# Kernel tuning notes

Measured on AMD Instinct MI355X. Metric: run time of the kernel, lower is better.

## Reference

```python
import jax, jax.numpy as jnp
import numpy as np

N_NODES = 100000
N_EDGES = 1200000
IN_FEATS = 64
OUT_FEATS = 64


def setup_inputs() -> dict:
    key = jax.random.key(0)
    k1, k2, k3, k4 = jax.random.split(key, 4)
    feature = jax.random.normal(k1, (N_NODES, IN_FEATS), dtype=jnp.float32)
    edge_src = jax.random.randint(k2, (N_EDGES,), 0, N_NODES, dtype=jnp.int32)
    edge_dst = jax.random.randint(k3, (N_EDGES,), 0, N_NODES, dtype=jnp.int32)
    # xavier_normal_ init for linear weight (fan_in=fan_out=64)
    std = float(np.sqrt(2.0 / (IN_FEATS + OUT_FEATS)))
    W = jax.random.normal(k4, (OUT_FEATS, IN_FEATS), dtype=jnp.float32) * std
    b = jnp.zeros((OUT_FEATS,), dtype=jnp.float32)
    return {"feature": feature, "edge_src": edge_src, "edge_dst": edge_dst, "W": W, "b": b}


def reference(feature, edge_src, edge_dst, W, b):
    # copy_src: gather source-node features per edge, then mean-reduce by dst.
    msgs = feature[edge_src]                                   # [E, d_in]
    summed = jax.ops.segment_sum(msgs, edge_dst, num_segments=N_NODES)  # [N, d_in]
    deg = jax.ops.segment_sum(jnp.ones((edge_src.shape[0],), feature.dtype),
                              edge_dst, num_segments=N_NODES)  # [N]
    h = summed / jnp.maximum(deg, 1.0)[:, None]                # mean; 0 for isolated nodes
    # apply_nodes: linear + activation
    h = jnp.einsum("nd,od->no", h, W) + b
    return jax.nn.relu(h)
```

## Files before the change

### kernel.cpp

```cpp
#include <hip/hip_runtime.h>


typedef __attribute__((ext_vector_type(8))) short short8;
typedef __attribute__((ext_vector_type(4))) float floatx4;

constexpr int kNodes = 100000;
constexpr int kEdges = 1200000;

constexpr int kBuckets = 1024;
constexpr int kBucketNodes = 98;

constexpr int kBinBlocks = 256;
constexpr int kEdgesPerBlock = 4688;
constexpr int kEPT = (kEdgesPerBlock + 1023) / 1024;

constexpr int kCap = 2048;
constexpr int kAccStride = 68;

constexpr int kWsFeat   = 0;
constexpr int kWsOff    = 3200000;
constexpr int kWsBinned = kWsOff + kBinBlocks * (kBuckets + 1);

__device__ __forceinline__ unsigned bf16rne(float f) {
  unsigned u = __float_as_uint(f);
  return (u + 0x7fffu + ((u >> 16) & 1u)) >> 16;
}

__global__ __launch_bounds__(1024) void gcn_build(
    const float* __restrict__ feat,
    const int* __restrict__ src, const int* __restrict__ dst,
    int* __restrict__ ws) {
  uint2* fb16 = (uint2*)(ws + kWsFeat);
  int* offT   = ws + kWsOff;
  int* binned = ws + kWsBinned;

  __shared__ int lhist[kBuckets];
  __shared__ int lcur[kBuckets];
  __shared__ int wsum[16];

  const int tid = threadIdx.x;
  lhist[tid] = 0;
  __syncthreads();

  const int e0 = blockIdx.x * kEdgesPerBlock;
  const int cnt = min(kEdgesPerBlock, kEdges - e0);
  int es[kEPT], ebk[kEPT], edl[kEPT];
  #pragma unroll
  for (int k = 0; k < kEPT; ++k) {
    const int j = tid + k * 1024;
    if (j < cnt) {
      es[k] = src[e0 + j];
      const int d = dst[e0 + j];
      const int bk = d / kBucketNodes;
      ebk[k] = bk;
      edl[k] = d - bk * kBucketNodes;
      atomicAdd(&lhist[bk], 1);
    }
  }

  const int t = blockIdx.x * 1024 + tid;
  for (int i = t; i < kNodes * 16; i += kBinBlocks * 1024) {
    const float* fr = feat + (size_t)(i >> 4) * 64 + (i & 15);
    uint2 p;
    p.x = bf16rne(fr[0])  | (bf16rne(fr[16]) << 16);
    p.y = bf16rne(fr[32]) | (bf16rne(fr[48]) << 16);
    fb16[i] = p;
  }
  __syncthreads();

  const int own = lhist[tid];
  const int wv = tid >> 6, ln = tid & 63;
  int sc = own;
  #pragma unroll
  for (int off = 1; off < 64; off <<= 1) {
    const int v = __shfl_up(sc, off, 64);
    if (ln >= off) sc += v;
  }
  if (ln == 63) wsum[wv] = sc;
  __syncthreads();
  if (tid < 64) {
    int tw = (tid < 16) ? wsum[tid] : 0;
    #pragma unroll
    for (int off = 1; off < 16; off <<= 1) {
      const int v = __shfl_up(tw, off, 64);
      if (tid >= off) tw += v;
    }
    if (tid < 16) wsum[tid] = tw;
  }
  __syncthreads();
  const int excl = sc - own + (wv ? wsum[wv - 1] : 0);
  lcur[tid] = excl;
  offT[blockIdx.x * (kBuckets + 1) + tid] = excl;
  if (tid == 0) offT[blockIdx.x * (kBuckets + 1) + kBuckets] = cnt;
  __syncthreads();

  int* myBin = binned + blockIdx.x * kEdgesPerBlock;
  #pragma unroll
  for (int k = 0; k < kEPT; ++k) {
    const int j = tid + k * 1024;
    if (j < cnt) {
      const int pos = atomicAdd(&lcur[ebk[k]], 1);
      myBin[pos] = es[k] | (edl[k] << 17);
    }
  }
}

__global__ __launch_bounds__(1024, 8) void gcn_aggregate(
    const int*   __restrict__ ws_in,
    const float* __restrict__ W,
    const float* __restrict__ b,
    float*       __restrict__ out) {
  const uint2* fb16 = (const uint2*)(ws_in + kWsFeat);
  const int* offT   = ws_in + kWsOff;
  const int* binned = ws_in + kWsBinned;

  __shared__ __align__(16) char uShared[112 * 72 * 2];
  __shared__ __align__(16) int accum[kBucketNodes * kAccStride];
  __shared__ int    lofs[129];
  __shared__ int    lcur[128];
  __shared__ int    slotR[65];
  __shared__ int    runL[kBinBlocks + 1];
  __shared__ int    runG[kBinBlocks];
  __shared__ int    ssm[kBinBlocks];
  __shared__ ushort Wb16[64 * 64];
  __shared__ float  bsh[64];
  int*    lsrc  = (int*)uShared;
  ushort* hsAll = (ushort*)uShared;

  const int tid = threadIdx.x;
  const int bkt = blockIdx.x;

  if (tid < 128) lcur[tid] = 0;
  for (int i = tid; i < 4096; i += 1024) Wb16[i] = (ushort)bf16rne(W[i]);
  if (tid < 64) bsh[tid] = b[tid];

  if (tid < kBinBlocks) {
    const int o0 = offT[tid * (kBuckets + 1) + bkt];
    const int o1 = offT[tid * (kBuckets + 1) + bkt + 1];
    ssm[tid] = o1 - o0;
    runG[tid] = tid * kEdgesPerBlock + o0;
  }
  __syncthreads();
  if (tid < 64) {
    const int base = tid * 4;
    const int v0 = ssm[base], v1 = ssm[base + 1];
    const int v2 = ssm[base + 2], v3 = ssm[base + 3];
    const int p1 = v0 + v1, p2 = p1 + v2, tot = p2 + v3;
    int sc = tot;
    #pragma unroll
    for (int off = 1; off < 64; off <<= 1) {
      const int v = __shfl_up(sc, off, 64);
      if (tid >= off) sc += v;
    }
    const int ex = sc - tot;
    runL[base]     = ex;
    runL[base + 1] = ex + v0;
    runL[base + 2] = ex + p1;
    runL[base + 3] = ex + p2;
    if (tid == 63) runL[kBinBlocks] = sc;
  }
  __syncthreads();

  int sz = runL[kBinBlocks];
  if (sz > kCap) sz = kCap;

  auto mapRead = [&](int j) -> unsigned {
    int lo = 0, hi = kBinBlocks;
    #pragma unroll
    for (int it = 0; it < 8; ++it) {
      const int mid = (lo + hi) >> 1;
      if (runL[mid] <= j) lo = mid; else hi = mid;
    }
    return (unsigned)binned[runG[lo] + (j - runL[lo])];
  };

  const int j0 = tid, j1 = tid + 1024;
  const bool va = j0 < sz, vb = j1 < sz;
  unsigned ea = 0, eb = 0;
  if (va) { ea = mapRead(j0); atomicAdd(&lcur[ea >> 17], 1); }
  if (vb) { eb = mapRead(j1); atomicAdd(&lcur[eb >> 17], 1); }
  __syncthreads();

  if (tid < 64) {
    const int a  = lcur[tid * 2];
    const int b2 = lcur[tid * 2 + 1];
    int s = a + b2;
    #pragma unroll
    for (int off = 1; off < 64; off <<= 1) {
      const int v = __shfl_up(s, off, 64);
      if (tid >= off) s += v;
    }
    const int ex1 = s - b2;
    const int ex0 = ex1 - a;
    lofs[tid * 2]     = ex0;
    lofs[tid * 2 + 1] = ex1;
    lcur[tid * 2]     = ex0;
    lcur[tid * 2 + 1] = ex1;
    if (tid == 63) lofs[128] = s;
  }
  __syncthreads();

  if (va) { const int p = atomicAdd(&lcur[ea >> 17], 1); lsrc[p] = (int)ea; }
  if (vb) { const int p = atomicAdd(&lcur[eb >> 17], 1); lsrc[p] = (int)eb; }
  if (tid < 64) {
    const int tgt = (sz * tid) >> 6;
    int lo = 0, hi = kBucketNodes;
    #pragma unroll
    for (int it = 0; it < 7; ++it) {
      const int mid = (lo + hi) >> 1;
      if (lofs[mid] < tgt) lo = mid + 1; else hi = mid;
    }
    slotR[tid] = lo;
  }
  if (tid == 64) slotR[64] = kBucketNodes;
  __syncthreads();

  const int wave = tid >> 6;
  const int lane = tid & 63;
  const int g = lane >> 4;
  const int c = lane & 15;
  {
    const int slot = wave * 4 + g;
    int r = slotR[slot];
    const int rEnd = slotR[slot + 1];
    if (r < rEnd) {
      int j = lofs[r];
      const int jE = lofs[rEnd];
      int jN = lofs[r + 1];
      float a0 = 0.f, a1 = 0.f, a2 = 0.f, a3 = 0.f;
      unsigned e = (j < jE) ? (unsigned)lsrc[j] : 0u;
      uint2 v = fb16[(size_t)(e & 0x1FFFF) * 16 + c];
      while (j < jE) {
        while (j >= jN) {
          int* rp = accum + r * kAccStride + c;
          rp[0]  = __float_as_int(a0);
          rp[16] = __float_as_int(a1);
          rp[32] = __float_as_int(a2);
          rp[48] = __float_as_int(a3);
          a0 = a1 = a2 = a3 = 0.f;
          ++r; jN = lofs[r + 1];
        }
        const int jn = j + 1;
        const unsigned e2 = (jn < jE) ? (unsigned)lsrc[jn] : 0u;
        const uint2 v2 = fb16[(size_t)(e2 & 0x1FFFF) * 16 + c];
        a0 += __uint_as_float(v.x << 16);
        a1 += __uint_as_float(v.x & 0xffff0000u);
        a2 += __uint_as_float(v.y << 16);
        a3 += __uint_as_float(v.y & 0xffff0000u);
        v = v2; e = e2; j = jn;
      }
      while (r < rEnd) {
        int* rp = accum + r * kAccStride + c;
        rp[0]  = __float_as_int(a0);
        rp[16] = __float_as_int(a1);
        rp[32] = __float_as_int(a2);
        rp[48] = __float_as_int(a3);
        a0 = a1 = a2 = a3 = 0.f;
        ++r;
      }
    }
  }
  __syncthreads();

  {
    const int nd = tid >> 3;
    const int ch = tid & 7;
    if (nd < kBucketNodes) {
      const int dg = lofs[nd + 1] - lofs[nd];
      const float inv = 1.0f / (float)(dg > 1 ? dg : 1);
      const int* arow = accum + nd * kAccStride + ch * 8;
      const int4 pa = *(const int4*)(arow);
      const int4 pb = *(const int4*)(arow + 4);
      unsigned h0 = bf16rne(__int_as_float(pa.x) * inv);
      unsigned h1 = bf16rne(__int_as_float(pa.y) * inv);
      unsigned h2 = bf16rne(__int_as_float(pa.z) * inv);
      unsigned h3 = bf16rne(__int_as_float(pa.w) * inv);
      unsigned h4 = bf16rne(__int_as_float(pb.x) * inv);
      unsigned h5 = bf16rne(__int_as_float(pb.y) * inv);
      unsigned h6 = bf16rne(__int_as_float(pb.z) * inv);
      unsigned h7 = bf16rne(__int_as_float(pb.w) * inv);
      uint4 pk;
      pk.x = h0 | (h1 << 16);
      pk.y = h2 | (h3 << 16);
      pk.z = h4 | (h5 << 16);
      pk.w = h6 | (h7 << 16);
      *(uint4*)(hsAll + nd * 72 + ch * 8) = pk;
    } else {
      if (nd < 112) *(uint4*)(hsAll + nd * 72 + ch * 8) =
          make_uint4(0u, 0u, 0u, 0u);
    }
  }
  __syncthreads();

  if (tid < 448) {
    const int w8   = tid >> 6;
    const int ln   = tid & 63;
    const int quad = ln >> 4;
    const int col  = ln & 15;
    const int n0 = bkt * kBucketNodes;

    const short8 af0 = *reinterpret_cast<const short8*>(
        hsAll + (w8 * 16 + col) * 72 + 0 * 32 + quad * 8);
    const short8 af1 = *reinterpret_cast<const short8*>(
        hsAll + (w8 * 16 + col) * 72 + 1 * 32 + quad * 8);

    #pragma unroll
    for (int ob = 0; ob < 4; ++ob) {
      const short8 bf0 = *reinterpret_cast<const short8*>(
          Wb16 + (ob * 16 + col) * 64 + 0 * 32 + quad * 8);
      const short8 bf1 = *reinterpret_cast<const short8*>(
          Wb16 + (ob * 16 + col) * 64 + 1 * 32 + quad * 8);
      floatx4 acc = {0.f, 0.f, 0.f, 0.f};
      acc = __builtin_amdgcn_mfma_f32_16x16x32_bf16(af0, bf0, acc, 0, 0, 0);
      acc = __builtin_amdgcn_mfma_f32_16x16x32_bf16(af1, bf1, acc, 0, 0, 0);

      const int o = ob * 16 + col;
      const float bo = bsh[o];
      #pragma unroll
      for (int r = 0; r < 4; ++r) {
        const int local = w8 * 16 + quad * 4 + r;
        const int node = n0 + local;
        if (local < kBucketNodes && node < kNodes) {
          const float v = acc[r] + bo;
          out[(size_t)node * 64 + o] = v > 0.0f ? v : 0.0f;
        }
      }
    }
  }
}

extern "C" void kernel_launch(void* const* d_in, const int* in_sizes, int n_in,
                              void* d_out, int out_size, void* d_ws, size_t ws_size,
                              hipStream_t stream) {
  const float* feature  = (const float*)d_in[0];
  const int*   edge_src = (const int*)  d_in[1];
  const int*   edge_dst = (const int*)  d_in[2];
  const float* W        = (const float*)d_in[3];
  const float* b        = (const float*)d_in[4];

  float* out = (float*)d_out;
  int*   ws  = (int*)d_ws;

  gcn_build<<<kBinBlocks, 1024, 0, stream>>>(feature, edge_src, edge_dst, ws);
  gcn_aggregate<<<kBuckets, 1024, 0, stream>>>(ws, W, b, out);
}
```

Before: 132.9 us.

## Transpose bucket offset table and unroll per-node gather by four edges

The per-block bucket offset table is stored bucket-major instead of block-major, so the aggregate kernel's 256 threads read contiguous offsets for their bucket instead of striding by 1025 ints. The aggregation loop becomes a per-node loop that issues four independent feature gathers at a time into separate accumulators, replacing the single-edge software-pipelined loop. This aims for more memory-level parallelism on the gathers and coalesced offset reads, at the cost of more registers and a scalar remainder loop for low-degree nodes.

```diff
diff --git a/kernel.cpp b/kernel.cpp
--- a/kernel.cpp
+++ b/kernel.cpp
@@ -19,7 +19,7 @@
 
 constexpr int kWsFeat   = 0;
 constexpr int kWsOff    = 3200000;
-constexpr int kWsBinned = kWsOff + kBinBlocks * (kBuckets + 1);
+constexpr int kWsBinned = kWsOff + (kBuckets + 1) * kBinBlocks;
 
 __device__ __forceinline__ unsigned bf16rne(float f) {
   unsigned u = __float_as_uint(f);
@@ -31,7 +31,7 @@
     const int* __restrict__ src, const int* __restrict__ dst,
     int* __restrict__ ws) {
   uint2* fb16 = (uint2*)(ws + kWsFeat);
-  int* offT   = ws + kWsOff;
+  int* offTT  = ws + kWsOff;
   int* binned = ws + kWsBinned;
 
   __shared__ int lhist[kBuckets];
@@ -90,8 +90,8 @@
   __syncthreads();
   const int excl = sc - own + (wv ? wsum[wv - 1] : 0);
   lcur[tid] = excl;
-  offT[blockIdx.x * (kBuckets + 1) + tid] = excl;
-  if (tid == 0) offT[blockIdx.x * (kBuckets + 1) + kBuckets] = cnt;
+  offTT[tid * kBinBlocks + blockIdx.x] = excl;
+  if (tid == 0) offTT[kBuckets * kBinBlocks + blockIdx.x] = cnt;
   __syncthreads();
 
   int* myBin = binned + blockIdx.x * kEdgesPerBlock;
@@ -111,7 +111,7 @@
     const float* __restrict__ b,
     float*       __restrict__ out) {
   const uint2* fb16 = (const uint2*)(ws_in + kWsFeat);
-  const int* offT   = ws_in + kWsOff;
+  const int* offTT  = ws_in + kWsOff;
   const int* binned = ws_in + kWsBinned;
 
   __shared__ __align__(16) char uShared[112 * 72 * 2];
@@ -135,8 +135,8 @@
   if (tid < 64) bsh[tid] = b[tid];
 
   if (tid < kBinBlocks) {
-    const int o0 = offT[tid * (kBuckets + 1) + bkt];
-    const int o1 = offT[tid * (kBuckets + 1) + bkt + 1];
+    const int o0 = offTT[bkt * kBinBlocks + tid];
+    const int o1 = offTT[(bkt + 1) * kBinBlocks + tid];
     ssm[tid] = o1 - o0;
     runG[tid] = tid * kEdgesPerBlock + o0;
   }
@@ -221,43 +221,56 @@
   const int c = lane & 15;
   {
     const int slot = wave * 4 + g;
-    int r = slotR[slot];
     const int rEnd = slotR[slot + 1];
-    if (r < rEnd) {
-      int j = lofs[r];
-      const int jE = lofs[rEnd];
-      int jN = lofs[r + 1];
-      float a0 = 0.f, a1 = 0.f, a2 = 0.f, a3 = 0.f;
-      unsigned e = (j < jE) ? (unsigned)lsrc[j] : 0u;
-      uint2 v = fb16[(size_t)(e & 0x1FFFF) * 16 + c];
-      while (j < jE) {
-        while (j >= jN) {
-          int* rp = accum + r * kAccStride + c;
-          rp[0]  = __float_as_int(a0);
-          rp[16] = __float_as_int(a1);
-          rp[32] = __float_as_int(a2);
-          rp[48] = __float_as_int(a3);
-          a0 = a1 = a2 = a3 = 0.f;
-          ++r; jN = lofs[r + 1];
-        }
-        const int jn = j + 1;
-        const unsigned e2 = (jn < jE) ? (unsigned)lsrc[jn] : 0u;
-        const uint2 v2 = fb16[(size_t)(e2 & 0x1FFFF) * 16 + c];
-        a0 += __uint_as_float(v.x << 16);
-        a1 += __uint_as_float(v.x & 0xffff0000u);
-        a2 += __uint_as_float(v.y << 16);
-        a3 += __uint_as_float(v.y & 0xffff0000u);
-        v = v2; e = e2; j = jn;
+    for (int r = slotR[slot]; r < rEnd; ++r) {
+      const int jA = lofs[r];
+      const int jB = lofs[r + 1];
+      float s00 = 0.f, s01 = 0.f, s02 = 0.f, s03 = 0.f;
+      float s10 = 0.f, s11 = 0.f, s12 = 0.f, s13 = 0.f;
+      float s20 = 0.f, s21 = 0.f, s22 = 0.f, s23 = 0.f;
+      float s30 = 0.f, s31 = 0.f, s32 = 0.f, s33 = 0.f;
+      int j = jA;
+      #pragma unroll 1
+      for (; j + 4 <= jB; j += 4) {
+        const unsigned e0 = (unsigned)lsrc[j];
+        const unsigned e1 = (unsigned)lsrc[j + 1];
+        const unsigned e2 = (unsigned)lsrc[j + 2];
+        const unsigned e3 = (unsigned)lsrc[j + 3];
+        const uint2 v0 = fb16[(size_t)(e0 & 0x1FFFFu) * 16 + c];
+        const uint2 v1 = fb16[(size_t)(e1 & 0x1FFFFu) * 16 + c];
+        const uint2 v2 = fb16[(size_t)(e2 & 0x1FFFFu) * 16 + c];
+        const uint2 v3 = fb16[(size_t)(e3 & 0x1FFFFu) * 16 + c];
+        s00 += __uint_as_float(v0.x << 16);
+        s01 += __uint_as_float(v0.x & 0xffff0000u);
+        s02 += __uint_as_float(v0.y << 16);
+        s03 += __uint_as_float(v0.y & 0xffff0000u);
+        s10 += __uint_as_float(v1.x << 16);
+        s11 += __uint_as_float(v1.x & 0xffff0000u);
+        s12 += __uint_as_float(v1.y << 16);
+        s13 += __uint_as_float(v1.y & 0xffff0000u);
+        s20 += __uint_as_float(v2.x << 16);
+        s21 += __uint_as_float(v2.x & 0xffff0000u);
+        s22 += __uint_as_float(v2.y << 16);
+        s23 += __uint_as_float(v2.y & 0xffff0000u);
+        s30 += __uint_as_float(v3.x << 16);
+        s31 += __uint_as_float(v3.x & 0xffff0000u);
+        s32 += __uint_as_float(v3.y << 16);
+        s33 += __uint_as_float(v3.y & 0xffff0000u);
       }
-      while (r < rEnd) {
-        int* rp = accum + r * kAccStride + c;
-        rp[0]  = __float_as_int(a0);
-        rp[16] = __float_as_int(a1);
-        rp[32] = __float_as_int(a2);
-        rp[48] = __float_as_int(a3);
-        a0 = a1 = a2 = a3 = 0.f;
-        ++r;
+      #pragma unroll 1
+      for (; j < jB; ++j) {
+        const unsigned e = (unsigned)lsrc[j];
+        const uint2 v = fb16[(size_t)(e & 0x1FFFFu) * 16 + c];
+        s00 += __uint_as_float(v.x << 16);
+        s01 += __uint_as_float(v.x & 0xffff0000u);
+        s02 += __uint_as_float(v.y << 16);
+        s03 += __uint_as_float(v.y & 0xffff0000u);
       }
+      int* rp = accum + r * kAccStride + c;
+      rp[0]  = __float_as_int((s00 + s10) + (s20 + s30));
+      rp[16] = __float_as_int((s01 + s11) + (s21 + s31));
+      rp[32] = __float_as_int((s02 + s12) + (s22 + s32));
+      rp[48] = __float_as_int((s03 + s13) + (s23 + s33));
     }
   }
   __syncthreads();
```

After: 137.7 us. +3.6%, slower.
